# Kernel optimization log

Measured on AMD Instinct MI355X. Metric: run time of the kernel, lower is better.

Reference implementation:

```python
import jax, jax.numpy as jnp
import numpy as np

HID = 2048
NKH, NVH = 16, 32
DK, DV = 128, 128
KCONV = 4
KEY_DIM = NKH * DK          # 2048
VAL_DIM = NVH * DV          # 4096
CONV_DIM = 2 * KEY_DIM + VAL_DIM  # 8192
QKVZ_DIM = 2 * KEY_DIM + 2 * VAL_DIM  # 12288
R = NVH // NKH              # 2
BA_DIM = 2 * NVH            # 64
EPS = 1e-6


def _l2norm(x, eps=1e-6):
    return x * jax.lax.rsqrt(jnp.sum(x * x, axis=-1, keepdims=True) + eps)


def setup_inputs() -> dict:
    key = jax.random.key(0)
    ks = jax.random.split(key, 8)
    std = 0.02
    return {
        "hidden_states": jax.random.normal(ks[0], (2, 2048, HID), dtype=jnp.float32),
        "attention_mask": jnp.ones((2, 2048), dtype=jnp.float32),
        "W_qkvz": jax.random.normal(ks[1], (HID, QKVZ_DIM), dtype=jnp.float32) * std,
        "W_ba": jax.random.normal(ks[2], (HID, BA_DIM), dtype=jnp.float32) * std,
        "conv_kernel": jax.random.normal(ks[3], (KCONV, 1, CONV_DIM), dtype=jnp.float32) * 0.1,
        "A_log": jnp.log(jax.random.uniform(ks[4], (NVH,), dtype=jnp.float32, minval=1.0, maxval=16.0)),
        "dt_bias": jnp.ones((NVH,), dtype=jnp.float32),
        "norm_kernel": jnp.ones((DV,), dtype=jnp.float32),
        "W_out": jax.random.normal(ks[5], (VAL_DIM, HID), dtype=jnp.float32) * std,
    }


def reference(hidden_states, attention_mask, W_qkvz, W_ba, conv_kernel, A_log, dt_bias, norm_kernel, W_out):
    b, s, _ = hidden_states.shape
    h = hidden_states * attention_mask[:, :, None]  # apply padding mask

    # projections
    qkvz = h @ W_qkvz  # (b, s, QKVZ_DIM)
    ba = h @ W_ba      # (b, s, BA_DIM)

    # fix_query_key_value_ordering: grouped per-k-head layout [q, k, v*R, z*R]
    qkvz = qkvz.reshape(b, s, NKH, 2 * DK + 2 * R * DV)
    q = qkvz[..., :DK]                                   # (b,s,NKH,DK)
    k = qkvz[..., DK:2 * DK]                             # (b,s,NKH,DK)
    v = qkvz[..., 2 * DK:2 * DK + R * DV].reshape(b, s, NVH, DV)
    z = qkvz[..., 2 * DK + R * DV:].reshape(b, s, NVH, DV)
    ba = ba.reshape(b, s, NKH, 2 * R)
    beta = ba[..., :R].reshape(b, s, NVH)
    alpha = ba[..., R:].reshape(b, s, NVH)

    # causal depthwise conv over [q|k|v] channels
    conv_in = jnp.concatenate(
        [q.reshape(b, s, -1), k.reshape(b, s, -1), v.reshape(b, s, -1)], axis=-1)  # (b,s,CONV_DIM)
    conv_out = jax.lax.conv_general_dilated(
        conv_in, conv_kernel, window_strides=(1,), padding=((KCONV - 1, 0),),
        dimension_numbers=("NWC", "WIO", "NWC"), feature_group_count=CONV_DIM)
    conv_out = jax.nn.silu(conv_out)

    q = conv_out[..., :KEY_DIM].reshape(b, s, NKH, DK)
    k = conv_out[..., KEY_DIM:2 * KEY_DIM].reshape(b, s, NKH, DK)
    v = conv_out[..., 2 * KEY_DIM:].reshape(b, s, NVH, DV)

    # expand k-heads to v-heads (repeat_interleave)
    q = jnp.repeat(q, R, axis=2)  # (b,s,NVH,DK)
    k = jnp.repeat(k, R, axis=2)

    # gated delta rule parameters
    g = -jnp.exp(A_log)[None, None, :] * jax.nn.softplus(alpha + dt_bias[None, None, :])  # (b,s,NVH)
    beta = jax.nn.sigmoid(beta)
    q = _l2norm(q) * (DK ** -0.5)
    k = _l2norm(k)

    # recurrence: S_t = exp(g_t) * S_{t-1} + k_t (v_t - k_t^T S) beta_t ; o_t = q_t^T S_t
    def step(S, x):
        q_t, k_t, v_t, g_t, b_t = x
        S = S * jnp.exp(g_t)[..., None, None]               # (b,h,DK,DV)
        kv = jnp.einsum("bhk,bhkv->bhv", k_t, S)
        delta = (v_t - kv) * b_t[..., None]
        S = S + jnp.einsum("bhk,bhv->bhkv", k_t, delta)
        o_t = jnp.einsum("bhk,bhkv->bhv", q_t, S)
        return S, o_t

    xs = (q.transpose(1, 0, 2, 3), k.transpose(1, 0, 2, 3), v.transpose(1, 0, 2, 3),
          g.transpose(1, 0, 2), beta.transpose(1, 0, 2))
    S0 = jnp.zeros((b, NVH, DK, DV), dtype=hidden_states.dtype)
    _, o = jax.lax.scan(step, S0, xs)
    o = o.transpose(1, 0, 2, 3)  # (b,s,NVH,DV)

    # gated RMSNorm per head (fp32 math as in Qwen3NextRMSNormGated)
    of = o.astype(jnp.float32)
    var = jnp.mean(of * of, axis=-1, keepdims=True)
    of = of * jax.lax.rsqrt(var + EPS)
    of = norm_kernel * of
    of = of * jax.nn.silu(z.astype(jnp.float32))
    o = of.astype(o.dtype).reshape(b, s, VAL_DIM)

    return o @ W_out
```

## Files before the change

### kernel.cpp

```cpp
#include <hip/hip_runtime.h>
#include <stdint.h>

typedef float    f32x4 __attribute__((ext_vector_type(4)));
typedef float    f32x2 __attribute__((ext_vector_type(2)));
typedef _Float16 f16x8 __attribute__((ext_vector_type(8)));
typedef _Float16 f16x4 __attribute__((ext_vector_type(4)));
typedef _Float16 f16x2 __attribute__((ext_vector_type(2)));

#define SEQ   2048
#define HIDD  2048
#define MROWS 4096
#define NQKV  12288
#define NCHUNK 32
#define CLEN   64

__device__ __forceinline__ void gload_lds16(const void* g, void* l) {
  __builtin_amdgcn_global_load_lds((const __attribute__((address_space(1))) uint32_t*)g,
                                   (__attribute__((address_space(3))) uint32_t*)l, 16, 0, 0);
}
__device__ __forceinline__ int swz256(int row, int colb) { return row * 256 + (colb ^ ((row & 7) << 4)); }
__device__ __forceinline__ int swz128(int row, int colb) { return row * 128 + (colb ^ ((row & 7) << 4)); }

__global__ __launch_bounds__(256)
void amask_kernel(const float* __restrict__ h, const float* __restrict__ mask,
                  _Float16* __restrict__ A1) {
  int i = blockIdx.x * 256 + threadIdx.x;
  if (i >= MROWS * HIDD / 4) return;
  f32x4 x = ((const f32x4*)h)[i];
  float m = mask[(i * 4) >> 11];
  f16x4 r;
  r[0] = (_Float16)(x[0] * m); r[1] = (_Float16)(x[1] * m);
  r[2] = (_Float16)(x[2] * m); r[3] = (_Float16)(x[3] * m);
  *(f16x4*)(A1 + (size_t)i * 4) = r;
}

__global__ __launch_bounds__(256)
void transpose_f16(const float* __restrict__ in, _Float16* __restrict__ out,
                   int R, int C) {
  __shared__ float tile[64][65];
  int c0 = blockIdx.x * 64, r0 = blockIdx.y * 64;
  int tx = threadIdx.x & 63, ty = threadIdx.x >> 6;
  #pragma unroll
  for (int i = 0; i < 16; ++i) {
    int r = i * 4 + ty;
    tile[r][tx] = in[(size_t)(r0 + r) * C + c0 + tx];
  }
  __syncthreads();
  #pragma unroll
  for (int i = 0; i < 16; ++i) {
    int c = i * 4 + ty;
    out[(size_t)(c0 + c) * R + r0 + tx] = (_Float16)tile[tx][c];
  }
}

template <typename CT>
__global__ __launch_bounds__(512, 2)
void gemm256(const _Float16* __restrict__ A, const _Float16* __restrict__ Bt,
             CT* __restrict__ C, int M, int N, int K, int tiles_n) {
  __shared__ __align__(16) _Float16 lsA[2][256 * 64];
  __shared__ __align__(16) _Float16 lsB[2][256 * 64];
  int bm = blockIdx.x / tiles_n, bn = blockIdx.x % tiles_n;
  int m0 = bm * 256, n0 = bn * 256;
  int tid = threadIdx.x;
  int w = tid >> 6, lane = tid & 63;
  int wm = w >> 2, wn = w & 3;
  int la = lane & 15, lk = lane >> 4;
  int sr = lane >> 3;
  int scb = ((lane & 7) << 4) ^ ((sr & 7) << 4);
  int nkt = K >> 6;
  f32x4 acc[8][4] = {};

  {
    const char* ga = (const char*)(A  + (size_t)(m0 + w * 32) * K);
    const char* gb = (const char*)(Bt + (size_t)(n0 + w * 32) * K);
    #pragma unroll
    for (int i = 0; i < 4; ++i) {
      gload_lds16(ga + (size_t)(i * 8 + sr) * (K * 2) + scb, &lsA[0][(w * 32 + i * 8) * 64]);
      gload_lds16(gb + (size_t)(i * 8 + sr) * (K * 2) + scb, &lsB[0][(w * 32 + i * 8) * 64]);
    }
  }
  __syncthreads();

  int cur = 0;
  for (int kt = 0; kt < nkt; ++kt) {
    if (kt + 1 < nkt) {
      const char* ga = (const char*)(A  + (size_t)(m0 + w * 32) * K + (kt + 1) * 64);
      const char* gb = (const char*)(Bt + (size_t)(n0 + w * 32) * K + (kt + 1) * 64);
      #pragma unroll
      for (int i = 0; i < 4; ++i) {
        gload_lds16(ga + (size_t)(i * 8 + sr) * (K * 2) + scb, &lsA[cur ^ 1][(w * 32 + i * 8) * 64]);
        gload_lds16(gb + (size_t)(i * 8 + sr) * (K * 2) + scb, &lsB[cur ^ 1][(w * 32 + i * 8) * 64]);
      }
    }
    const char* cA = (const char*)&lsA[cur][0];
    const char* cB = (const char*)&lsB[cur][0];
    #pragma unroll
    for (int kw = 0; kw < 2; ++kw) {
      f16x8 af[8], bf[4];
      #pragma unroll
      for (int f = 0; f < 8; ++f) {
        int row = wm * 128 + f * 16 + la;
        af[f] = *(const f16x8*)(cA + row * 128 + ((kw * 64 + lk * 16) ^ ((row & 7) << 4)));
      }
      #pragma unroll
      for (int j = 0; j < 4; ++j) {
        int row = wn * 64 + j * 16 + la;
        bf[j] = *(const f16x8*)(cB + row * 128 + ((kw * 64 + lk * 16) ^ ((row & 7) << 4)));
      }
      #pragma unroll
      for (int f = 0; f < 8; ++f)
        #pragma unroll
        for (int j = 0; j < 4; ++j)
          acc[f][j] = __builtin_amdgcn_mfma_f32_16x16x32_f16(af[f], bf[j], acc[f][j], 0, 0, 0);
    }
    __syncthreads();
    cur ^= 1;
  }

  #pragma unroll
  for (int f = 0; f < 8; ++f)
    #pragma unroll
    for (int j = 0; j < 4; ++j) {
      int col = n0 + wn * 64 + j * 16 + la;
      #pragma unroll
      for (int r = 0; r < 4; ++r) {
        int row = m0 + wm * 128 + f * 16 + lk * 4 + r;
        C[(size_t)row * N + col] = (CT)acc[f][j][r];
      }
    }
}

__global__ __launch_bounds__(256)
void ba_gemm(const float* __restrict__ h, const float* __restrict__ mask,
             const float* __restrict__ Wba, float* __restrict__ ba) {
  __shared__ float red[4][8][64];
  int r0 = blockIdx.x * 8;
  int c = threadIdx.x & 63, kc = threadIdx.x >> 6;
  float acc[8] = {};
  const float* wp = Wba + (size_t)(kc * 512) * 64 + c;
  const float* hp = h + (size_t)r0 * HIDD + kc * 512;
  for (int i = 0; i < 512; ++i) {
    float w = wp[(size_t)i * 64];
    #pragma unroll
    for (int r = 0; r < 8; ++r)
      acc[r] += hp[(size_t)r * HIDD + i] * w;
  }
  #pragma unroll
  for (int r = 0; r < 8; ++r) red[kc][r][c] = acc[r];
  __syncthreads();
  if (kc == 0) {
    #pragma unroll
    for (int r = 0; r < 8; ++r) {
      float s = red[0][r][c] + red[1][r][c] + red[2][r][c] + red[3][r][c];
      ba[(size_t)(r0 + r) * 64 + c] = s * mask[r0 + r];
    }
  }
}

__global__ __launch_bounds__(256)
void conv_kernel(const _Float16* __restrict__ qkvz, const float* __restrict__ ck,
                 _Float16* __restrict__ qn, _Float16* __restrict__ kn,
                 _Float16* __restrict__ vb) {
  int row = blockIdx.x;
  int b = row >> 11, t = row & 2047;
  int lane = threadIdx.x & 63, wid = threadIdx.x >> 6;
  for (int u = wid; u < 64; u += 4) {
    int c, cc, hh;
    if (u < 16)      { hh = u;      c = hh * 768;                               cc = hh * 128; }
    else if (u < 32) { hh = u - 16; c = hh * 768 + 128;                         cc = 2048 + hh * 128; }
    else             { hh = u - 32; c = (hh >> 1) * 768 + 256 + (hh & 1) * 128; cc = 4096 + hh * 128; }
    float y0 = 0.f, y1 = 0.f;
    #pragma unroll
    for (int j = 0; j < 4; ++j) {
      int tt = t - 3 + j;
      if (tt >= 0) {
        const _Float16* r = qkvz + (size_t)(b * 2048 + tt) * NQKV + c;
        f16x2 x = *(const f16x2*)(r + 2 * lane);
        f32x2 w = *(const f32x2*)(ck + j * 8192 + cc + 2 * lane);
        y0 += (float)x[0] * w[0];
        y1 += (float)x[1] * w[1];
      }
    }
    y0 = y0 / (1.f + expf(-y0));
    y1 = y1 / (1.f + expf(-y1));
    if (u < 32) {
      float ss = y0 * y0 + y1 * y1;
      #pragma unroll
      for (int m = 1; m < 64; m <<= 1) ss += __shfl_xor(ss, m);
      float rs = rsqrtf(ss + 1e-6f);
      if (u < 16) rs *= 0.08838834764831845f;
      y0 *= rs; y1 *= rs;
      _Float16* dst = (u < 16 ? qn : kn) + (size_t)row * 2048 + hh * 128;
      f16x2 o; o[0] = (_Float16)y0; o[1] = (_Float16)y1;
      *(f16x2*)(dst + 2 * lane) = o;
    } else {
      _Float16* dst = vb + (size_t)row * 4096 + hh * 128;
      f16x2 o; o[0] = (_Float16)y0; o[1] = (_Float16)y1;
      *(f16x2*)(dst + 2 * lane) = o;
    }
  }
}

__global__ __launch_bounds__(256)
void egbeta_kernel(const float* __restrict__ ba, const float* __restrict__ Alog,
                   const float* __restrict__ dtb, float* __restrict__ gout,
                   float* __restrict__ bout) {
  int i = blockIdx.x * 256 + threadIdx.x;
  if (i >= MROWS * 32) return;
  int vh = i >> 12, row = i & 4095;
  int kh = vh >> 1, r = vh & 1;
  const float* p = ba + (size_t)row * 64 + kh * 4;
  float bv = p[r], av = p[2 + r];
  float x = av + dtb[vh];
  float sp = (x > 20.f) ? x : log1pf(expf(x));
  gout[(size_t)vh * MROWS + row] = -expf(Alog[vh]) * sp;
  bout[(size_t)vh * MROWS + row] = 1.f / (1.f + expf(-bv));
}

__global__ __launch_bounds__(512, 2)
void chunk_scan(const _Float16* __restrict__ qn, const _Float16* __restrict__ kn,
                _Float16* __restrict__ vb, const float* __restrict__ gb,
                const float* __restrict__ btb) {
  __shared__ __align__(16) _Float16 Ks[64 * 128];
  __shared__ __align__(16) _Float16 Qs[64 * 128];
  __shared__ __align__(16) _Float16 Kt[128 * 64];
  __shared__ __align__(16) _Float16 Sf[32 * 128];
  __shared__ float AT[64 * 65];
  __shared__ __align__(16) _Float16 M16[64 * 64];
  __shared__ float RHS[32 * 65];
  __shared__ __align__(16) _Float16 Uv[32 * 64];
  __shared__ __align__(16) _Float16 Ub[32 * 64];
  __shared__ __align__(16) _Float16 Vb[64 * 32];
  __shared__ float gs[64], bs[64], cgs[64], bexp[64], scU[64];

  char* Ksb = (char*)Ks; char* Qsb = (char*)Qs; char* Ktb = (char*)Kt;
  char* Sfb = (char*)Sf; char* M16b = (char*)M16;
  char* Uvb = (char*)Uv; char* Ubb = (char*)Ub; char* Vbb = (char*)Vb;

  int bid = blockIdx.x;
  int b = bid >> 7, vh = (bid >> 2) & 31, vsl = bid & 3;
  int kh = vh >> 1;
  int tid = threadIdx.x;
  int w = tid >> 6, lane = tid & 63;
  int wr = w >> 1, wc = w & 1;
  int la = lane & 15, lk = lane >> 4;

  const _Float16* kgb = kn + (size_t)(b * 2048) * 2048 + kh * 128;
  const _Float16* qgb = qn + (size_t)(b * 2048) * 2048 + kh * 128;
  _Float16*       vgb = vb + (size_t)(b * 2048) * 4096 + vh * 128 + vsl * 32;
  const float*    ggb = gb  + (size_t)vh * MROWS + b * 2048;
  const float*    bgb = btb + (size_t)vh * MROWS + b * 2048;

  int srow = tid >> 3, sseg = tid & 7;
  int tk = tid & 127, tth = tid >> 7;

  f16x8 kr[2], qr[2]; f16x4 vr; float ebr;
  float sreg[2][4] = {};

  { f32x4 z = {}; ((f32x4*)Sf)[tid] = z; }

  kr[0] = *(const f16x8*)(kgb + (size_t)srow * 2048 + sseg * 16);
  kr[1] = *(const f16x8*)(kgb + (size_t)srow * 2048 + sseg * 16 + 8);
  qr[0] = *(const f16x8*)(qgb + (size_t)srow * 2048 + sseg * 16);
  qr[1] = *(const f16x8*)(qgb + (size_t)srow * 2048 + sseg * 16 + 8);
  vr    = *(const f16x4*)(vgb + (size_t)srow * 4096 + sseg * 4);
  ebr   = (tid < 64) ? ggb[tid] : (tid < 128 ? bgb[tid - 64] : 0.f);
  *(f16x8*)(Ksb + swz256(srow, sseg * 32))      = kr[0];
  *(f16x8*)(Ksb + swz256(srow, sseg * 32 + 16)) = kr[1];
  *(f16x8*)(Qsb + swz256(srow, sseg * 32))      = qr[0];
  *(f16x8*)(Qsb + swz256(srow, sseg * 32 + 16)) = qr[1];
  *(f16x4*)(Vbb + srow * 64 + sseg * 8) = vr;
  if (tid < 64) gs[tid] = ebr; else if (tid < 128) bs[tid - 64] = ebr;
  __syncthreads();

  #pragma unroll 1
  for (int c = 0; c < NCHUNK; ++c) {
    int cn = (c < NCHUNK - 1) ? c + 1 : c;
    kr[0] = *(const f16x8*)(kgb + (size_t)(cn * 64 + srow) * 2048 + sseg * 16);
    kr[1] = *(const f16x8*)(kgb + (size_t)(cn * 64 + srow) * 2048 + sseg * 16 + 8);
    qr[0] = *(const f16x8*)(qgb + (size_t)(cn * 64 + srow) * 2048 + sseg * 16);
    qr[1] = *(const f16x8*)(qgb + (size_t)(cn * 64 + srow) * 2048 + sseg * 16 + 8);
    vr    = *(const f16x4*)(vgb + (size_t)(cn * 64 + srow) * 4096 + sseg * 4);
    ebr   = (tid < 64) ? ggb[cn * 64 + tid] : (tid < 128 ? bgb[cn * 64 + tid - 64] : 0.f);

    f32x4 kk[2] = {}, qk[2] = {}, ks0 = {}, qs0 = {};
    #pragma unroll
    for (int ks = 0; ks < 4; ++ks) {
      f16x8 aK = *(const f16x8*)(Ksb + swz256(wr * 16 + la, ks * 64 + lk * 16));
      f16x8 aQ = *(const f16x8*)(Qsb + swz256(wr * 16 + la, ks * 64 + lk * 16));
      f16x8 bS = *(const f16x8*)(Sfb + swz256(wc * 16 + la, ks * 64 + lk * 16));
      #pragma unroll
      for (int j = 0; j < 2; ++j) {
        f16x8 bK = *(const f16x8*)(Ksb + swz256(wc * 32 + j * 16 + la, ks * 64 + lk * 16));
        kk[j] = __builtin_amdgcn_mfma_f32_16x16x32_f16(aK, bK, kk[j], 0, 0, 0);
        qk[j] = __builtin_amdgcn_mfma_f32_16x16x32_f16(aQ, bK, qk[j], 0, 0, 0);
      }
      ks0 = __builtin_amdgcn_mfma_f32_16x16x32_f16(aK, bS, ks0, 0, 0, 0);
      qs0 = __builtin_amdgcn_mfma_f32_16x16x32_f16(aQ, bS, qs0, 0, 0, 0);
    }
    {
      f16x8 r0, r1;
      #pragma unroll
      for (int j = 0; j < 8; ++j) {
        r0[j] = *(const _Float16*)(Ksb + swz256(tth * 16 + j, 2 * tk));
        r1[j] = *(const _Float16*)(Ksb + swz256(tth * 16 + 8 + j, 2 * tk));
      }
      *(f16x8*)(Ktb + swz128(tk, tth * 32))      = r0;
      *(f16x8*)(Ktb + swz128(tk, tth * 32 + 16)) = r1;
    }
    if (w == 0) {
      float g = gs[lane];
      #pragma unroll
      for (int off = 1; off < 64; off <<= 1) {
        float y = __shfl_up(g, off);
        if (lane >= off) g += y;
      }
      cgs[lane] = g;
      float cgL = __shfl(g, 63);
      bexp[lane] = __expf(g);
      scU[lane] = bs[lane] * __expf(cgL - g);
    }
    __syncthreads();

    {
      float cgt[4];
      #pragma unroll
      for (int r = 0; r < 4; ++r) cgt[r] = cgs[wr * 16 + lk * 4 + r];
      #pragma unroll
      for (int j = 0; j < 2; ++j) {
        int s = wc * 32 + j * 16 + la;
        float bsv = bs[s], cgss = cgs[s];
        #pragma unroll
        for (int r = 0; r < 4; ++r) {
          int t = wr * 16 + lk * 4 + r;
          float e = bsv * __expf(cgt[r] - cgss);
          AT[s * 65 + t] = (s < t) ? e * kk[j][r] : 0.f;
          float mm = (s <= t) ? e * qk[j][r] : 0.f;
          *(_Float16*)(M16b + swz128(t, s * 2)) = (_Float16)mm;
        }
      }
      #pragma unroll
      for (int r = 0; r < 4; ++r) {
        int t = wr * 16 + lk * 4 + r;
        int v = wc * 16 + la;
        float be = bexp[t];
        qs0[r] *= be;
        float vv = (float)*(const _Float16*)(Vbb + t * 64 + v * 2);
        RHS[v * 65 + t] = vv - be * ks0[r];
      }
    }
    __syncthreads();

    {
      float u[4];
      #pragma unroll
      for (int vi = 0; vi < 4; ++vi) u[vi] = RHS[(w * 4 + vi) * 65 + lane];
      #pragma unroll 1
      for (int sb = 0; sb < 8; ++sb) {
        float Ac[8];
        #pragma unroll
        for (int j = 0; j < 8; ++j) Ac[j] = AT[(sb * 8 + j) * 65 + lane];
        #pragma unroll
        for (int j = 0; j < 8; ++j) {
          int s = sb * 8 + j;
          #pragma unroll
          for (int vi = 0; vi < 4; ++vi) {
            float ubv = __builtin_bit_cast(float,
                __builtin_amdgcn_readlane(__builtin_bit_cast(int, u[vi]), s));
            u[vi] = fmaf(-Ac[j], ubv, u[vi]);
          }
        }
      }
      float sc = scU[lane];
      #pragma unroll
      for (int vi = 0; vi < 4; ++vi) {
        int v = w * 4 + vi;
        *(_Float16*)(Uvb + swz128(v, lane * 2)) = (_Float16)u[vi];
        *(_Float16*)(Ubb + swz128(v, lane * 2)) = (_Float16)(u[vi] * sc);
      }
    }
    __syncthreads();

    #pragma unroll
    for (int ss = 0; ss < 2; ++ss) {
      f16x8 aM = *(const f16x8*)(M16b + swz128(wr * 16 + la, ss * 64 + lk * 16));
      f16x8 bU = *(const f16x8*)(Uvb + swz128(wc * 16 + la, ss * 64 + lk * 16));
      qs0 = __builtin_amdgcn_mfma_f32_16x16x32_f16(aM, bU, qs0, 0, 0, 0);
    }
    #pragma unroll
    for (int r = 0; r < 4; ++r) {
      int t = wr * 16 + lk * 4 + r;
      vgb[(size_t)(c * 64 + t) * 4096 + wc * 16 + la] = (_Float16)qs0[r];
    }
    {
      f32x4 sd[2] = {};
      #pragma unroll
      for (int ss = 0; ss < 2; ++ss) {
        f16x8 bK = *(const f16x8*)(Ktb + swz128(w * 16 + la, ss * 64 + lk * 16));
        #pragma unroll
        for (int vt = 0; vt < 2; ++vt) {
          f16x8 aU = *(const f16x8*)(Ubb + swz128(vt * 16 + la, ss * 64 + lk * 16));
          sd[vt] = __builtin_amdgcn_mfma_f32_16x16x32_f16(aU, bK, sd[vt], 0, 0, 0);
        }
      }
      float beC = bexp[63];
      #pragma unroll
      for (int vt = 0; vt < 2; ++vt)
        #pragma unroll
        for (int r = 0; r < 4; ++r) {
          int v = vt * 16 + lk * 4 + r;
          int k = w * 16 + la;
          float sn = fmaf(sreg[vt][r], beC, sd[vt][r]);
          sreg[vt][r] = sn;
          *(_Float16*)(Sfb + swz256(v, k * 2)) = (_Float16)sn;
        }
    }
    __syncthreads();

    *(f16x8*)(Ksb + swz256(srow, sseg * 32))      = kr[0];
    *(f16x8*)(Ksb + swz256(srow, sseg * 32 + 16)) = kr[1];
    *(f16x8*)(Qsb + swz256(srow, sseg * 32))      = qr[0];
    *(f16x8*)(Qsb + swz256(srow, sseg * 32 + 16)) = qr[1];
    *(f16x4*)(Vbb + srow * 64 + sseg * 8) = vr;
    if (tid < 64) gs[tid] = ebr; else if (tid < 128) bs[tid - 64] = ebr;
    __syncthreads();
  }
}

__global__ __launch_bounds__(256)
void gate_kernel(const _Float16* __restrict__ ob, const _Float16* __restrict__ qkvz,
                 const float* __restrict__ nk, _Float16* __restrict__ Ag) {
  int row = blockIdx.x;
  int lane = threadIdx.x & 63, wid = threadIdx.x >> 6;
  for (int vh = wid; vh < 32; vh += 4) {
    const _Float16* op = ob + (size_t)row * 4096 + vh * 128;
    f16x2 xx = *(const f16x2*)(op + 2 * lane);
    float x0 = (float)xx[0], x1 = (float)xx[1];
    float ss = x0 * x0 + x1 * x1;
    #pragma unroll
    for (int m = 1; m < 64; m <<= 1) ss += __shfl_xor(ss, m);
    float rs = rsqrtf(ss * (1.f / 128.f) + 1e-6f);
    f32x2 nv = *(const f32x2*)(nk + 2 * lane);
    float v0 = x0 * rs * nv[0], v1 = x1 * rs * nv[1];
    const _Float16* zp = qkvz + (size_t)row * NQKV + (vh >> 1) * 768 + 512 + (vh & 1) * 128;
    f16x2 zz = *(const f16x2*)(zp + 2 * lane);
    float z0 = (float)zz[0], z1 = (float)zz[1];
    v0 *= z0 / (1.f + expf(-z0));
    v1 *= z1 / (1.f + expf(-z1));
    _Float16* dst = Ag + (size_t)row * 4096 + vh * 128;
    f16x2 o; o[0] = (_Float16)v0; o[1] = (_Float16)v1;
    *(f16x2*)(dst + 2 * lane) = o;
  }
}

extern "C" void kernel_launch(void* const* d_in, const int* in_sizes, int n_in,
                              void* d_out, int out_size, void* d_ws, size_t ws_size,
                              hipStream_t stream) {
  const float* h     = (const float*)d_in[0];
  const float* mask  = (const float*)d_in[1];
  const float* Wqkvz = (const float*)d_in[2];
  const float* Wba   = (const float*)d_in[3];
  const float* ck    = (const float*)d_in[4];
  const float* Alog  = (const float*)d_in[5];
  const float* dtb   = (const float*)d_in[6];
  const float* nk    = (const float*)d_in[7];
  const float* Wout  = (const float*)d_in[8];
  float* out = (float*)d_out;

  char* w = (char*)d_ws;
  const size_t o_qkvz = 0;
  const size_t o_A1   = 100663296;
  const size_t o_Bt1  = o_A1 + 16777216;
  const size_t o_ba   = o_Bt1 + 50331648;
  const size_t o_g    = o_ba + 1048576;
  const size_t o_bt   = o_g + 524288;
  const size_t total  = o_bt + 524288;
  if (ws_size < total) return;

  _Float16* qkvz16 = (_Float16*)(w + o_qkvz);
  _Float16* A1     = (_Float16*)(w + o_A1);
  _Float16* Bt1    = (_Float16*)(w + o_Bt1);
  float*    ba32   = (float*)   (w + o_ba);
  float*    gbuf   = (float*)   (w + o_g);
  float*    btb    = (float*)   (w + o_bt);
  _Float16* qn16 = (_Float16*)(w + o_A1);
  _Float16* kn16 = (_Float16*)(w + o_Bt1);
  _Float16* vb16 = (_Float16*)(w + o_Bt1 + 16777216);
  _Float16* Ag   = (_Float16*)(w + o_A1);
  _Float16* Wt2  = (_Float16*)(w + 0);

  amask_kernel<<<MROWS * HIDD / 4 / 256, 256, 0, stream>>>(h, mask, A1);
  transpose_f16<<<dim3(192, 32), 256, 0, stream>>>(Wqkvz, Bt1, HIDD, NQKV);
  ba_gemm<<<MROWS / 8, 256, 0, stream>>>(h, mask, Wba, ba32);
  gemm256<_Float16><<<16 * 48, 512, 0, stream>>>(A1, Bt1, qkvz16, MROWS, NQKV, HIDD, 48);
  conv_kernel<<<MROWS, 256, 0, stream>>>(qkvz16, ck, qn16, kn16, vb16);
  egbeta_kernel<<<MROWS * 32 / 256, 256, 0, stream>>>(ba32, Alog, dtb, gbuf, btb);
  chunk_scan<<<256, 512, 0, stream>>>(qn16, kn16, vb16, gbuf, btb);
  gate_kernel<<<MROWS, 256, 0, stream>>>(vb16, qkvz16, nk, Ag);
  transpose_f16<<<dim3(32, 64), 256, 0, stream>>>(Wout, Wt2, 4096, HIDD);
  gemm256<float><<<16 * 8, 512, 0, stream>>>(Ag, Wt2, out, MROWS, HIDD, 4096, 8);
}
```

Before: 744.7 us.

## Prefetch two K-tiles ahead in GEMM and use 128-row tiles for output projection

Rewrites the GEMM pipeline so global-to-LDS loads run two K-steps ahead, with an explicit vmcnt wait and raw barriers replacing the load-then-syncthreads pattern. This lets load latency overlap with more MFMA work. The kernel is also templated on the M tile size, and the output projection now uses 128-row tiles, doubling its grid from 128 to 256 blocks to fill more compute units. The risks are the hand-counted vmcnt threshold and buffer-reuse ordering, and that smaller tiles give less data reuse.

```diff
diff --git a/kernel.cpp b/kernel.cpp
--- a/kernel.cpp
+++ b/kernel.cpp
@@ -53,14 +53,18 @@
   }
 }
 
-template <typename CT>
+template <typename CT, int BM>
 __global__ __launch_bounds__(512, 2)
-void gemm256(const _Float16* __restrict__ A, const _Float16* __restrict__ Bt,
+void gemm2ph(const _Float16* __restrict__ A, const _Float16* __restrict__ Bt,
              CT* __restrict__ C, int M, int N, int K, int tiles_n) {
-  __shared__ __align__(16) _Float16 lsA[2][256 * 64];
+  constexpr int RF  = BM / 32;
+  constexpr int AR  = BM / 8;
+  constexpr int NA  = AR / 8;
+  constexpr int STG = NA + 4;
+  __shared__ __align__(16) _Float16 lsA[2][BM * 64];
   __shared__ __align__(16) _Float16 lsB[2][256 * 64];
   int bm = blockIdx.x / tiles_n, bn = blockIdx.x % tiles_n;
-  int m0 = bm * 256, n0 = bn * 256;
+  int m0 = bm * BM, n0 = bn * 256;
   int tid = threadIdx.x;
   int w = tid >> 6, lane = tid & 63;
   int wm = w >> 2, wn = w & 3;
@@ -68,38 +72,35 @@
   int sr = lane >> 3;
   int scb = ((lane & 7) << 4) ^ ((sr & 7) << 4);
   int nkt = K >> 6;
-  f32x4 acc[8][4] = {};
-
-  {
-    const char* ga = (const char*)(A  + (size_t)(m0 + w * 32) * K);
-    const char* gb = (const char*)(Bt + (size_t)(n0 + w * 32) * K);
-    #pragma unroll
-    for (int i = 0; i < 4; ++i) {
-      gload_lds16(ga + (size_t)(i * 8 + sr) * (K * 2) + scb, &lsA[0][(w * 32 + i * 8) * 64]);
-      gload_lds16(gb + (size_t)(i * 8 + sr) * (K * 2) + scb, &lsB[0][(w * 32 + i * 8) * 64]);
-    }
-  }
-  __syncthreads();
+  f32x4 acc[RF][4] = {};
+
+  auto stage = [&](int kt, int buf) {
+    const char* ga = (const char*)(A  + (size_t)(m0 + w * AR) * K + kt * 64);
+    const char* gb = (const char*)(Bt + (size_t)(n0 + w * 32) * K + kt * 64);
+    #pragma unroll
+    for (int i = 0; i < NA; ++i)
+      gload_lds16(ga + (size_t)(i * 8 + sr) * (K * 2) + scb, &lsA[buf][(w * AR + i * 8) * 64]);
+    #pragma unroll
+    for (int i = 0; i < 4; ++i)
+      gload_lds16(gb + (size_t)(i * 8 + sr) * (K * 2) + scb, &lsB[buf][(w * 32 + i * 8) * 64]);
+  };
+
+  stage(0, 0);
+  if (nkt > 1) stage(1, 1);
 
   int cur = 0;
   for (int kt = 0; kt < nkt; ++kt) {
-    if (kt + 1 < nkt) {
-      const char* ga = (const char*)(A  + (size_t)(m0 + w * 32) * K + (kt + 1) * 64);
-      const char* gb = (const char*)(Bt + (size_t)(n0 + w * 32) * K + (kt + 1) * 64);
-      #pragma unroll
-      for (int i = 0; i < 4; ++i) {
-        gload_lds16(ga + (size_t)(i * 8 + sr) * (K * 2) + scb, &lsA[cur ^ 1][(w * 32 + i * 8) * 64]);
-        gload_lds16(gb + (size_t)(i * 8 + sr) * (K * 2) + scb, &lsB[cur ^ 1][(w * 32 + i * 8) * 64]);
-      }
-    }
+    if (kt < nkt - 1) asm volatile("s_waitcnt vmcnt(%0)" :: "i"(STG) : "memory");
+    else              asm volatile("s_waitcnt vmcnt(0)" ::: "memory");
+    __builtin_amdgcn_s_barrier();
     const char* cA = (const char*)&lsA[cur][0];
     const char* cB = (const char*)&lsB[cur][0];
     #pragma unroll
     for (int kw = 0; kw < 2; ++kw) {
-      f16x8 af[8], bf[4];
-      #pragma unroll
-      for (int f = 0; f < 8; ++f) {
-        int row = wm * 128 + f * 16 + la;
+      f16x8 af[RF], bf[4];
+      #pragma unroll
+      for (int f = 0; f < RF; ++f) {
+        int row = wm * (BM / 2) + f * 16 + la;
         af[f] = *(const f16x8*)(cA + row * 128 + ((kw * 64 + lk * 16) ^ ((row & 7) << 4)));
       }
       #pragma unroll
@@ -108,23 +109,24 @@
         bf[j] = *(const f16x8*)(cB + row * 128 + ((kw * 64 + lk * 16) ^ ((row & 7) << 4)));
       }
       #pragma unroll
-      for (int f = 0; f < 8; ++f)
+      for (int f = 0; f < RF; ++f)
         #pragma unroll
         for (int j = 0; j < 4; ++j)
           acc[f][j] = __builtin_amdgcn_mfma_f32_16x16x32_f16(af[f], bf[j], acc[f][j], 0, 0, 0);
     }
-    __syncthreads();
+    __builtin_amdgcn_s_barrier();
+    if (kt + 2 < nkt) stage(kt + 2, cur);
     cur ^= 1;
   }
 
   #pragma unroll
-  for (int f = 0; f < 8; ++f)
+  for (int f = 0; f < RF; ++f)
     #pragma unroll
     for (int j = 0; j < 4; ++j) {
       int col = n0 + wn * 64 + j * 16 + la;
       #pragma unroll
       for (int r = 0; r < 4; ++r) {
-        int row = m0 + wm * 128 + f * 16 + lk * 4 + r;
+        int row = m0 + wm * (BM / 2) + f * 16 + lk * 4 + r;
         C[(size_t)row * N + col] = (CT)acc[f][j][r];
       }
     }
@@ -492,11 +494,11 @@
   amask_kernel<<<MROWS * HIDD / 4 / 256, 256, 0, stream>>>(h, mask, A1);
   transpose_f16<<<dim3(192, 32), 256, 0, stream>>>(Wqkvz, Bt1, HIDD, NQKV);
   ba_gemm<<<MROWS / 8, 256, 0, stream>>>(h, mask, Wba, ba32);
-  gemm256<_Float16><<<16 * 48, 512, 0, stream>>>(A1, Bt1, qkvz16, MROWS, NQKV, HIDD, 48);
+  gemm2ph<_Float16, 256><<<16 * 48, 512, 0, stream>>>(A1, Bt1, qkvz16, MROWS, NQKV, HIDD, 48);
   conv_kernel<<<MROWS, 256, 0, stream>>>(qkvz16, ck, qn16, kn16, vb16);
   egbeta_kernel<<<MROWS * 32 / 256, 256, 0, stream>>>(ba32, Alog, dtb, gbuf, btb);
   chunk_scan<<<256, 512, 0, stream>>>(qn16, kn16, vb16, gbuf, btb);
   gate_kernel<<<MROWS, 256, 0, stream>>>(vb16, qkvz16, nk, Ag);
   transpose_f16<<<dim3(32, 64), 256, 0, stream>>>(Wout, Wt2, 4096, HIDD);
-  gemm256<float><<<16 * 8, 512, 0, stream>>>(Ag, Wt2, out, MROWS, HIDD, 4096, 8);
-}
+  gemm2ph<float, 128><<<32 * 8, 512, 0, stream>>>(Ag, Wt2, out, MROWS, HIDD, 4096, 8);
+}
```

Result: faster. 700.2 us (-6.0%).
